# Performance work log

Measured on AMD Instinct MI355X. Metric: run time of the kernel, lower is better.

Reference implementation:

```python
import jax, jax.numpy as jnp
import numpy as np

NUM_NODES = 200000
B = 65536          # n_id batch size
E = 131072         # events per direction
D_MEM = 128
D_RAW = 128
D_TIME = 128
T_MAX = 1000000


def setup_inputs() -> dict:
    key = jax.random.key(0)
    ks = jax.random.split(key, 16)
    inp = {
        'memory': jax.random.normal(ks[0], (NUM_NODES, D_MEM), jnp.float32),
        'last_update': jax.random.randint(ks[1], (NUM_NODES,), 0, 1000, jnp.int64),
        'n_id': jnp.arange(B, dtype=jnp.int64),
        'src_s': jax.random.randint(ks[2], (E,), 0, B, jnp.int64),
        'dst_s': jax.random.randint(ks[3], (E,), 0, B, jnp.int64),
        't_s': jax.random.randint(ks[4], (E,), 0, T_MAX, jnp.int64),
        'raw_msg_s': jax.random.normal(ks[5], (E, D_RAW), jnp.float32),
        'src_d': jax.random.randint(ks[6], (E,), 0, B, jnp.int64),
        'dst_d': jax.random.randint(ks[7], (E,), 0, B, jnp.int64),
        't_d': jax.random.randint(ks[8], (E,), 0, T_MAX, jnp.int64),
        'raw_msg_d': jax.random.normal(ks[9], (E, D_RAW), jnp.float32),
        'w_time': jax.random.normal(ks[10], (D_TIME, 1), jnp.float32) * 0.1,
        'b_time': jax.random.normal(ks[11], (D_TIME,), jnp.float32) * 0.1,
        'W_ih': jax.random.normal(ks[12], (3 * D_MEM, 2 * D_MEM + D_RAW + D_TIME), jnp.float32) * 0.05,
        'W_hh': jax.random.normal(ks[13], (3 * D_MEM, D_MEM), jnp.float32) * 0.05,
        'b_ih': jax.random.normal(ks[14], (3 * D_MEM,), jnp.float32) * 0.05,
        'b_hh': jax.random.normal(ks[15], (3 * D_MEM,), jnp.float32) * 0.05,
    }
    return inp


def _time_enc(t_rel, w_time, b_time):
    # Linear(1, time_dim) followed by cos: cos(t * w + b)
    return jnp.cos(t_rel.astype(jnp.float32)[:, None] * w_time[:, 0][None, :] + b_time)


def reference(memory, last_update, n_id, src_s, dst_s, t_s, raw_msg_s,
              src_d, dst_d, t_d, raw_msg_d, w_time, b_time, W_ih, W_hh, b_ih, b_hh):
    nb = n_id.shape[0]
    # assoc: global node id -> local index within n_id
    assoc = jnp.zeros((memory.shape[0],), dtype=jnp.int32).at[n_id].set(
        jnp.arange(nb, dtype=jnp.int32))

    # source-side messages (IdentityMessage = concat)
    t_enc_s = _time_enc(t_s - last_update[src_s], w_time, b_time)
    msg_s = jnp.concatenate([memory[src_s], memory[dst_s], raw_msg_s, t_enc_s], axis=-1)

    # destination-side messages
    t_enc_d = _time_enc(t_d - last_update[dst_d], w_time, b_time)
    msg_d = jnp.concatenate([memory[dst_d], memory[src_d], raw_msg_d, t_enc_d], axis=-1)

    idx = jnp.concatenate([src_s, dst_d], axis=0)       # [2E] global ids
    msg = jnp.concatenate([msg_s, msg_d], axis=0)       # [2E, 512]
    t = jnp.concatenate([t_s, t_d], axis=0)             # [2E]
    loc = assoc[idx]                                     # [2E] local ids

    # LastAggregator: per local node, pick the message with max t (ties -> latest position)
    ne = t.shape[0]
    key = t * ne + jnp.arange(ne, dtype=t.dtype)         # encode (t, position)
    maxkey = jax.ops.segment_max(key, loc, num_segments=nb)
    count = jax.ops.segment_sum(jnp.ones_like(loc), loc, num_segments=nb)
    has = count > 0
    argm = jnp.where(has, maxkey % ne, 0)
    aggr = jnp.where(has[:, None], msg[argm], 0.0)       # [nb, 512]

    # GRUCell(x=aggr, h=memory[n_id])
    h = memory[n_id]
    gi = aggr @ W_ih.T + b_ih
    gh = h @ W_hh.T + b_hh
    gi_r, gi_z, gi_n = jnp.split(gi, 3, axis=-1)
    gh_r, gh_z, gh_n = jnp.split(gh, 3, axis=-1)
    r = jax.nn.sigmoid(gi_r + gh_r)
    z = jax.nn.sigmoid(gi_z + gh_z)
    n = jnp.tanh(gi_n + r * gh_n)
    new_memory = (1.0 - z) * n + z * h

    new_last_update = last_update.at[idx].set(t)[n_id]
    return new_memory, new_last_update
```

## Files before the change

### kernel.cpp

```cpp
#include <hip/hip_runtime.h>
#include <math.h>

#define NB        65536
#define EV        131072
#define NE        (2*EV)
#define DM        128
#define NO2       512
#define BM        64
#define THREADS   512
#define SWZ(r)    ((((r) ^ ((r) >> 2))) & 3)

typedef float f32x4 __attribute__((ext_vector_type(4)));
typedef long  longx2 __attribute__((ext_vector_type(2)));
typedef unsigned long long u64;

__device__ __forceinline__ float fcos_rev(float rev) {
    float r; asm("v_cos_f32 %0, %1" : "=v"(r) : "v"(rev)); return r;
}
__device__ __forceinline__ float fexp2(float x) {
    float r; asm("v_exp_f32 %0, %1" : "=v"(r) : "v"(x)); return r;
}
__device__ __forceinline__ float frcp(float x) {
    float r; asm("v_rcp_f32 %0, %1" : "=v"(r) : "v"(x)); return r;
}
__device__ __forceinline__ float fast_cos(float arg) {
    double rv = (double)arg * 0.15915494309189535;
    rv -= floor(rv);
    return fcos_rev((float)rv);
}
__device__ __forceinline__ float fsigmoid(float x) {
    x = fminf(fmaxf(x, -30.f), 30.f);
    float e = fexp2(-1.44269504088896f * x);
    return frcp(1.f + e);
}
__device__ __forceinline__ float ftanh_(float x) {
    x = fminf(fmaxf(x, -15.f), 15.f);
    float e = fexp2(-2.88539008177793f * x);
    return (1.f - e) * frcp(1.f + e);
}

#if defined(__has_builtin) && __has_builtin(__builtin_amdgcn_cvt_pk_fp8_f32)
__device__ __forceinline__ unsigned pack4_fp8(float f0, float f1, float f2, float f3) {
    int v = __builtin_amdgcn_cvt_pk_fp8_f32(f0, f1, 0, false);
    v = __builtin_amdgcn_cvt_pk_fp8_f32(f2, f3, v, true);
    return (unsigned)v;
}
#else
__device__ __forceinline__ unsigned enc1_fp8(float x) {
    unsigned u = __float_as_uint(x);
    unsigned s = (u >> 24) & 0x80u;
    float a = fabsf(x);
    if (!(a >= 0.001953125f)) return s;
    if (a > 448.f) a = 448.f;
    int e; float mf = frexpf(a, &e);
    int E = e + 6, mant;
    if (E <= 0) {
        mant = (int)(a * 512.f + 0.5f);
        if (mant > 7) return s | 0x08u;
        return s | (unsigned)mant;
    }
    mant = (int)((mf * 2.f - 1.f) * 8.f + 0.5f);
    if (mant == 8) { mant = 0; ++E; }
    if (E > 15) { E = 15; mant = 6; }
    if (E == 15 && mant == 7) mant = 6;
    return s | (unsigned)(E << 3) | (unsigned)mant;
}
__device__ __forceinline__ unsigned pack4_fp8(float f0, float f1, float f2, float f3) {
    return enc1_fp8(f0) | (enc1_fp8(f1) << 8) | (enc1_fp8(f2) << 16) | (enc1_fp8(f3) << 24);
}
#endif

__global__ void prep_k(const int* __restrict__ src_s, const int* __restrict__ t_s,
                       const int* __restrict__ dst_d, const int* __restrict__ t_d,
                       u64* __restrict__ keyarr, u64* __restrict__ lukey,
                       const float* __restrict__ W_ih, const float* __restrict__ W_hh,
                       const float* __restrict__ b_ih, const float* __restrict__ b_hh,
                       unsigned char* __restrict__ wp8, float* __restrict__ bp) {
    int bid = blockIdx.x;
    if (bid < NE / 256) {
        int e = bid * 256 + threadIdx.x;
        int g, t;
        if (e < EV) { g = src_s[e];      t = t_s[e]; }
        else        { g = dst_d[e - EV]; t = t_d[e - EV]; }
        u64 key = ((u64)(unsigned)t << 18) + (u64)(unsigned)e + 1ull;
        atomicMax(&keyarr[g], key);
        u64 lk = ((u64)(unsigned)(e + 1) << 20) | (u64)(unsigned)t;
        atomicMax(&lukey[g], lk);
        return;
    }
    int idx = (bid - NE / 256) * 256 + threadIdx.x;
    int col = idx / 80, g = idx - col * 80;
    int step = g >> 3, sl = g & 7;
    int kg = ((sl >> 1) ^ SWZ(col)) + ((sl & 1) << 2);
    int k0 = step * 64 + kg * 8;
    int d = col >> 2, gate = col & 3;
    float f[8];
    #pragma unroll
    for (int j = 0; j < 8; ++j) {
        int c = k0 + j;
        float v = 0.f;
        if (c < 512) {
            int row = (gate == 0) ? d : (gate == 1) ? 128 + d : (gate == 2) ? 256 + d : -1;
            if (row >= 0) v = W_ih[(size_t)row * 512 + c];
        } else {
            int ch = c - 512;
            int row = (gate == 0) ? d : (gate == 1) ? 128 + d : (gate == 3) ? 256 + d : -1;
            if (row >= 0) v = W_hh[(size_t)row * 128 + ch];
        }
        f[j] = v * 16.f;
    }
    unsigned lo = pack4_fp8(f[0], f[1], f[2], f[3]);
    unsigned hi = pack4_fp8(f[4], f[5], f[6], f[7]);
    *(u64*)(wp8 + (size_t)step * 32768 + (size_t)col * 64 + (size_t)sl * 8)
        = (u64)lo | ((u64)hi << 32);
    if (g == 0) {
        float bv = (gate == 0) ? b_ih[d] + b_hh[d]
                 : (gate == 1) ? b_ih[128 + d] + b_hh[128 + d]
                 : (gate == 2) ? b_ih[256 + d] : b_hh[256 + d];
        bp[col] = bv;
    }
}

__global__ __launch_bounds__(THREADS, 4) void gemm_gru_k(
    const float* __restrict__ memory, const int* __restrict__ last_update,
    const int* __restrict__ src_s, const int* __restrict__ dst_s,
    const int* __restrict__ t_s, const float* __restrict__ raw_s,
    const int* __restrict__ src_d, const int* __restrict__ dst_d,
    const int* __restrict__ t_d, const float* __restrict__ raw_d,
    const float* __restrict__ w_time, const float* __restrict__ b_time,
    const unsigned char* __restrict__ wp8, const float* __restrict__ bp,
    const u64* __restrict__ keyarr, const u64* __restrict__ lukey,
    float* __restrict__ out_mem, float* __restrict__ out_lu)
{
    __shared__ __align__(16) char smem[74752];
    unsigned char* sA = (unsigned char*)smem;
    unsigned char* sB = (unsigned char*)(smem + 8192);
    float* sW = (float*)(smem + 73728);
    float* sBt= (float*)(smem + 74240);

    const int tid = threadIdx.x;
    const int m0  = blockIdx.x * BM;
    const int ln  = tid & 63, wn = tid >> 6;
    const int l2  = ln >> 4, rl = ln & 15;

    if (tid < DM) { sW[tid] = w_time[tid]; sBt[tid] = b_time[tid]; }

    const int ar = tid >> 3, ac = tid & 7;
    const int m  = m0 + ar;
    const u64 kk = keyarr[m];
    const int rv = (kk != 0ull);
    int a_ = 0, b_ = 0, t_ = 0;
    const float* pR = raw_s;
    if (kk) {
        int e = (int)((kk - 1ull) & (u64)(NE - 1));
        if (e < EV) { a_ = src_s[e]; b_ = dst_s[e]; t_ = t_s[e]; pR = raw_s + (size_t)e * DM; }
        else { int e2 = e - EV; a_ = dst_d[e2]; b_ = src_d[e2]; t_ = t_d[e2]; pR = raw_d + (size_t)e2 * DM; }
    }
    const float rt = rv ? (float)(t_ - last_update[a_]) : 0.f;
    const float* pA = memory + (size_t)a_ * DM;
    const float* pB = memory + (size_t)b_ * DM;
    const float* pH = memory + (size_t)m  * DM;

    float4 pv0, pv1;
    auto PREF_A = [&](int step) {
        int seg = step >> 1;
        if (seg == 3) return;
        const float* base = (seg == 0) ? pA : (seg == 1) ? pB : (seg == 2) ? pR : pH;
        int off = ((step & 1) << 6) + (ac << 3);
        pv0 = *(const float4*)(base + off);
        pv1 = *(const float4*)(base + off + 4);
    };
    auto STAGE_B = [&](int step, int buf) {
        const unsigned char* src = wp8 + (size_t)step * 32768 + (size_t)tid * 16;
        unsigned char* dst = sB + (size_t)buf * 32768 + (size_t)tid * 16;
        #pragma unroll
        for (int i = 0; i < 4; ++i)
            __builtin_amdgcn_global_load_lds(
                (const __attribute__((address_space(1))) void*)(src + i * 8192),
                (__attribute__((address_space(3))) void*)(dst + i * 8192), 16, 0, 0);
    };
    auto WRITE_A = [&](int step, int buf) {
        int seg = step >> 1;
        float f0, f1, f2, f3, f4, f5, f6, f7;
        if (seg == 3) {
            int coff = ((step & 1) << 6) + (ac << 3);
            f0 = fast_cos(__fadd_rn(__fmul_rn(rt, sW[coff+0]), sBt[coff+0]));
            f1 = fast_cos(__fadd_rn(__fmul_rn(rt, sW[coff+1]), sBt[coff+1]));
            f2 = fast_cos(__fadd_rn(__fmul_rn(rt, sW[coff+2]), sBt[coff+2]));
            f3 = fast_cos(__fadd_rn(__fmul_rn(rt, sW[coff+3]), sBt[coff+3]));
            f4 = fast_cos(__fadd_rn(__fmul_rn(rt, sW[coff+4]), sBt[coff+4]));
            f5 = fast_cos(__fadd_rn(__fmul_rn(rt, sW[coff+5]), sBt[coff+5]));
            f6 = fast_cos(__fadd_rn(__fmul_rn(rt, sW[coff+6]), sBt[coff+6]));
            f7 = fast_cos(__fadd_rn(__fmul_rn(rt, sW[coff+7]), sBt[coff+7]));
        } else {
            f0 = pv0.x; f1 = pv0.y; f2 = pv0.z; f3 = pv0.w;
            f4 = pv1.x; f5 = pv1.y; f6 = pv1.z; f7 = pv1.w;
        }
        if (seg < 4 && !rv) { f0=f1=f2=f3=f4=f5=f6=f7 = 0.f; }
        unsigned lo = pack4_fp8(f0, f1, f2, f3);
        unsigned hi = pack4_fp8(f4, f5, f6, f7);
        u64 q = (u64)lo | ((u64)hi << 32);
        *(u64*)(sA + buf * 4096 + ar * 64 + (((ac & 3) ^ SWZ(ar)) << 4) + ((ac >> 2) << 3)) = q;
    };

    f32x4 acc[4][4];
    #pragma unroll
    for (int mf = 0; mf < 4; ++mf)
        #pragma unroll
        for (int nf = 0; nf < 4; ++nf)
            acc[mf][nf] = (f32x4){0.f, 0.f, 0.f, 0.f};

    PREF_A(0);
    WRITE_A(0, 0);
    STAGE_B(0, 0);
    PREF_A(1);
    asm volatile("s_waitcnt vmcnt(2) lgkmcnt(0)" ::: "memory");
    __builtin_amdgcn_sched_barrier(0);
    __builtin_amdgcn_s_barrier();

    #pragma unroll
    for (int k = 0; k < 10; ++k) {
        const int cur = k & 1, nxt = cur ^ 1;

        longx2 a2[4], b2[4];
        #pragma unroll
        for (int mf = 0; mf < 4; ++mf) {
            int r = mf * 16 + rl;
            a2[mf] = *(const longx2*)(sA + cur * 4096 + r * 64 + ((l2 ^ SWZ(r)) << 4));
        }
        #pragma unroll
        for (int nf = 0; nf < 4; ++nf) {
            int c = wn * 64 + nf * 16 + rl;
            b2[nf] = *(const longx2*)(sB + cur * 32768 + c * 64 + ((l2 ^ SWZ(c)) << 4));
        }
        __builtin_amdgcn_sched_barrier(0);

        const bool pf = (k < 8) && (((k + 2) >> 1) != 3);
        if (k < 9) {
            WRITE_A(k + 1, nxt);
            __builtin_amdgcn_sched_barrier(0);
            STAGE_B(k + 1, nxt);
            __builtin_amdgcn_sched_barrier(0);
            if (pf) PREF_A(k + 2);
            __builtin_amdgcn_sched_barrier(0);
        }

        __builtin_amdgcn_s_setprio(1);
        #pragma unroll
        for (int mf = 0; mf < 4; ++mf)
            #pragma unroll
            for (int nf = 0; nf < 4; ++nf)
                acc[mf][nf] = __builtin_amdgcn_mfma_f32_16x16x32_fp8_fp8(
                    a2[mf].x, b2[nf].x, acc[mf][nf], 0, 0, 0);
        #pragma unroll
        for (int mf = 0; mf < 4; ++mf)
            #pragma unroll
            for (int nf = 0; nf < 4; ++nf)
                acc[mf][nf] = __builtin_amdgcn_mfma_f32_16x16x32_fp8_fp8(
                    a2[mf].y, b2[nf].y, acc[mf][nf], 0, 0, 0);
        __builtin_amdgcn_s_setprio(0);

        if (k < 9) {
            __builtin_amdgcn_sched_barrier(0);
            if (pf) asm volatile("s_waitcnt vmcnt(2) lgkmcnt(0)" ::: "memory");
            else    asm volatile("s_waitcnt vmcnt(0) lgkmcnt(0)" ::: "memory");
            __builtin_amdgcn_sched_barrier(0);
            __builtin_amdgcn_s_barrier();
        }
    }

    if (tid < BM) {
        u64 lk = lukey[m0 + tid];
        out_lu[m0 + tid] = lk ? (float)(unsigned)(lk & 0xFFFFFull)
                              : (float)last_update[m0 + tid];
    }
    __syncthreads();

    float* ep = (float*)(smem + wn * 4352);
    const int row16 = ln >> 2, dgrp = ln & 3;
    const int dbase = wn * 16 + dgrp * 4;
    const float ds = 0.0625f;
    f32x4 bb0 = *(const f32x4*)(bp + (dbase + 0) * 4);
    f32x4 bb1 = *(const f32x4*)(bp + (dbase + 1) * 4);
    f32x4 bb2 = *(const f32x4*)(bp + (dbase + 2) * 4);
    f32x4 bb3 = *(const f32x4*)(bp + (dbase + 3) * 4);

    #pragma unroll
    for (int mf = 0; mf < 4; ++mf) {
        #pragma unroll
        for (int nf = 0; nf < 4; ++nf)
            #pragma unroll
            for (int j = 0; j < 4; ++j)
                ep[((ln >> 4) * 4 + j) * 68 + nf * 16 + rl] = acc[mf][nf][j] * ds;
        asm volatile("s_waitcnt lgkmcnt(0)" ::: "memory");

        const int gm = m0 + mf * 16 + row16;
        const float* gr = ep + row16 * 68 + dgrp * 16;
        f32x4 g0 = *(const f32x4*)(gr + 0);
        f32x4 g1 = *(const f32x4*)(gr + 4);
        f32x4 g2 = *(const f32x4*)(gr + 8);
        f32x4 g3 = *(const f32x4*)(gr + 12);
        f32x4 h  = *(const f32x4*)(memory + (size_t)gm * DM + dbase);
        f32x4 res;
        {
            float rg = fsigmoid(g0.x + bb0.x);
            float zg = fsigmoid(g0.y + bb0.y);
            float ng = ftanh_(g0.z + bb0.z + rg * (g0.w + bb0.w));
            res.x = (1.f - zg) * ng + zg * h.x;
        }
        {
            float rg = fsigmoid(g1.x + bb1.x);
            float zg = fsigmoid(g1.y + bb1.y);
            float ng = ftanh_(g1.z + bb1.z + rg * (g1.w + bb1.w));
            res.y = (1.f - zg) * ng + zg * h.y;
        }
        {
            float rg = fsigmoid(g2.x + bb2.x);
            float zg = fsigmoid(g2.y + bb2.y);
            float ng = ftanh_(g2.z + bb2.z + rg * (g2.w + bb2.w));
            res.z = (1.f - zg) * ng + zg * h.z;
        }
        {
            float rg = fsigmoid(g3.x + bb3.x);
            float zg = fsigmoid(g3.y + bb3.y);
            float ng = ftanh_(g3.z + bb3.z + rg * (g3.w + bb3.w));
            res.w = (1.f - zg) * ng + zg * h.w;
        }
        *(f32x4*)(out_mem + (size_t)gm * DM + dbase) = res;
        if (mf < 3) asm volatile("s_waitcnt lgkmcnt(0)" ::: "memory");
    }
}

extern "C" void kernel_launch(void* const* d_in, const int* in_sizes, int n_in,
                              void* d_out, int out_size, void* d_ws, size_t ws_size,
                              hipStream_t stream) {
    const float* memory      = (const float*)d_in[0];
    const int*   last_update = (const int*)d_in[1];
    const int*   src_s       = (const int*)d_in[3];
    const int*   dst_s       = (const int*)d_in[4];
    const int*   t_s         = (const int*)d_in[5];
    const float* raw_s       = (const float*)d_in[6];
    const int*   src_d       = (const int*)d_in[7];
    const int*   dst_d       = (const int*)d_in[8];
    const int*   t_d         = (const int*)d_in[9];
    const float* raw_d       = (const float*)d_in[10];
    const float* w_time      = (const float*)d_in[11];
    const float* b_time      = (const float*)d_in[12];
    const float* W_ih        = (const float*)d_in[13];
    const float* W_hh        = (const float*)d_in[14];
    const float* b_ih        = (const float*)d_in[15];
    const float* b_hh        = (const float*)d_in[16];

    char* ws = (char*)d_ws;
    u64* keyarr = (u64*)ws;
    u64* lukey  = (u64*)(ws + 524288);
    unsigned char* wp8 = (unsigned char*)(ws + 1048576);
    float* bp = (float*)(ws + 1376256);

    hipMemsetAsync(d_ws, 0, 1048576, stream);

    prep_k<<<NE / 256 + (NO2 * 80) / 256, 256, 0, stream>>>(
        src_s, t_s, dst_d, t_d, keyarr, lukey, W_ih, W_hh, b_ih, b_hh, wp8, bp);

    float* out_mem = (float*)d_out;
    float* out_lu  = out_mem + (size_t)NB * DM;
    gemm_gru_k<<<NB / BM, THREADS, 0, stream>>>(memory, last_update,
        src_s, dst_s, t_s, raw_s, src_d, dst_d, t_d, raw_d,
        w_time, b_time, wp8, bp, keyarr, lukey, out_mem, out_lu);
}
```

Baseline: 79.29 us.

## Halve GEMM K-step and triple-buffer LDS with fragment prefetch

The fused GEMM+GRU kernel now moves through K in 32-wide fp8 steps (20 iterations) instead of 64-wide ones (10 iterations). The weight packing, swizzle and LDS layout are rewritten to match, and A/B tiles rotate through three LDS buffers. Fragments for the next step are read into registers before each barrier, so the MFMAs of one step overlap with staging two steps ahead. This cuts the LDS footprint and aims to hide load latency, but it doubles the number of block barriers and halves the MFMA work between them.

```diff
diff --git a/kernel.cpp b/kernel.cpp
--- a/kernel.cpp
+++ b/kernel.cpp
@@ -7,11 +7,10 @@
 #define DM        128
 #define NO2       512
 #define BM        64
+#define NST       20
 #define THREADS   512
-#define SWZ(r)    ((((r) ^ ((r) >> 2))) & 3)
 
 typedef float f32x4 __attribute__((ext_vector_type(4)));
-typedef long  longx2 __attribute__((ext_vector_type(2)));
 typedef unsigned long long u64;
 
 __device__ __forceinline__ float fcos_rev(float rev) {
@@ -90,9 +89,9 @@
     }
     int idx = (bid - NE / 256) * 256 + threadIdx.x;
     int col = idx / 80, g = idx - col * 80;
-    int step = g >> 3, sl = g & 7;
-    int kg = ((sl >> 1) ^ SWZ(col)) + ((sl & 1) << 2);
-    int k0 = step * 64 + kg * 8;
+    int step = g >> 2, sl = g & 3;
+    int kg = sl ^ ((col >> 2) & 3);
+    int k0 = step * 32 + kg * 8;
     int d = col >> 2, gate = col & 3;
     float f[8];
     #pragma unroll
@@ -111,7 +110,7 @@
     }
     unsigned lo = pack4_fp8(f[0], f[1], f[2], f[3]);
     unsigned hi = pack4_fp8(f[4], f[5], f[6], f[7]);
-    *(u64*)(wp8 + (size_t)step * 32768 + (size_t)col * 64 + (size_t)sl * 8)
+    *(u64*)(wp8 + (size_t)step * 16384 + (size_t)col * 32 + (size_t)sl * 8)
         = (u64)lo | ((u64)hi << 32);
     if (g == 0) {
         float bv = (gate == 0) ? b_ih[d] + b_hh[d]
@@ -132,11 +131,11 @@
     const u64* __restrict__ keyarr, const u64* __restrict__ lukey,
     float* __restrict__ out_mem, float* __restrict__ out_lu)
 {
-    __shared__ __align__(16) char smem[74752];
+    __shared__ __align__(16) char smem[56320];
     unsigned char* sA = (unsigned char*)smem;
-    unsigned char* sB = (unsigned char*)(smem + 8192);
-    float* sW = (float*)(smem + 73728);
-    float* sBt= (float*)(smem + 74240);
+    unsigned char* sB = (unsigned char*)(smem + 6144);
+    float* sW = (float*)(smem + 55296);
+    float* sBt= (float*)(smem + 55808);
 
     const int tid = threadIdx.x;
     const int m0  = blockIdx.x * BM;
@@ -161,46 +160,51 @@
     const float* pB = memory + (size_t)b_ * DM;
     const float* pH = memory + (size_t)m  * DM;
 
-    float4 pv0, pv1;
+    float4 pv;
     auto PREF_A = [&](int step) {
-        int seg = step >> 1;
+        int seg = step >> 2;
         if (seg == 3) return;
         const float* base = (seg == 0) ? pA : (seg == 1) ? pB : (seg == 2) ? pR : pH;
-        int off = ((step & 1) << 6) + (ac << 3);
-        pv0 = *(const float4*)(base + off);
-        pv1 = *(const float4*)(base + off + 4);
+        pv = *(const float4*)(base + ((step & 3) << 5) + (ac << 2));
     };
     auto STAGE_B = [&](int step, int buf) {
-        const unsigned char* src = wp8 + (size_t)step * 32768 + (size_t)tid * 16;
-        unsigned char* dst = sB + (size_t)buf * 32768 + (size_t)tid * 16;
-        #pragma unroll
-        for (int i = 0; i < 4; ++i)
-            __builtin_amdgcn_global_load_lds(
-                (const __attribute__((address_space(1))) void*)(src + i * 8192),
-                (__attribute__((address_space(3))) void*)(dst + i * 8192), 16, 0, 0);
+        const unsigned char* src = wp8 + (size_t)step * 16384 + (size_t)tid * 16;
+        unsigned char* dst = sB + (size_t)buf * 16384 + (size_t)tid * 16;
+        __builtin_amdgcn_global_load_lds((const __attribute__((address_space(1))) void*)src,
+            (__attribute__((address_space(3))) void*)dst, 16, 0, 0);
+        __builtin_amdgcn_global_load_lds((const __attribute__((address_space(1))) void*)(src + 8192),
+            (__attribute__((address_space(3))) void*)(dst + 8192), 16, 0, 0);
     };
     auto WRITE_A = [&](int step, int buf) {
-        int seg = step >> 1;
-        float f0, f1, f2, f3, f4, f5, f6, f7;
+        int seg = step >> 2;
+        float f0, f1, f2, f3;
         if (seg == 3) {
-            int coff = ((step & 1) << 6) + (ac << 3);
+            int coff = ((step & 3) << 5) + (ac << 2);
             f0 = fast_cos(__fadd_rn(__fmul_rn(rt, sW[coff+0]), sBt[coff+0]));
             f1 = fast_cos(__fadd_rn(__fmul_rn(rt, sW[coff+1]), sBt[coff+1]));
             f2 = fast_cos(__fadd_rn(__fmul_rn(rt, sW[coff+2]), sBt[coff+2]));
             f3 = fast_cos(__fadd_rn(__fmul_rn(rt, sW[coff+3]), sBt[coff+3]));
-            f4 = fast_cos(__fadd_rn(__fmul_rn(rt, sW[coff+4]), sBt[coff+4]));
-            f5 = fast_cos(__fadd_rn(__fmul_rn(rt, sW[coff+5]), sBt[coff+5]));
-            f6 = fast_cos(__fadd_rn(__fmul_rn(rt, sW[coff+6]), sBt[coff+6]));
-            f7 = fast_cos(__fadd_rn(__fmul_rn(rt, sW[coff+7]), sBt[coff+7]));
         } else {
-            f0 = pv0.x; f1 = pv0.y; f2 = pv0.z; f3 = pv0.w;
-            f4 = pv1.x; f5 = pv1.y; f6 = pv1.z; f7 = pv1.w;
-        }
-        if (seg < 4 && !rv) { f0=f1=f2=f3=f4=f5=f6=f7 = 0.f; }
-        unsigned lo = pack4_fp8(f0, f1, f2, f3);
-        unsigned hi = pack4_fp8(f4, f5, f6, f7);
-        u64 q = (u64)lo | ((u64)hi << 32);
-        *(u64*)(sA + buf * 4096 + ar * 64 + (((ac & 3) ^ SWZ(ar)) << 4) + ((ac >> 2) << 3)) = q;
+            f0 = pv.x; f1 = pv.y; f2 = pv.z; f3 = pv.w;
+        }
+        if (seg < 4 && !rv) { f0 = f1 = f2 = f3 = 0.f; }
+        unsigned q = pack4_fp8(f0, f1, f2, f3);
+        *(unsigned*)(sA + buf * 2048 + ar * 32
+                     + ((((ac >> 1) ^ ((ar >> 2) & 3)) << 3) + ((ac & 1) << 2))) = q;
+    };
+
+    long afr[4], bfr[4];
+    auto READ_FRAGS = [&](int buf) {
+        #pragma unroll
+        for (int mf = 0; mf < 4; ++mf) {
+            int r = mf * 16 + rl;
+            afr[mf] = *(const long*)(sA + buf * 2048 + r * 32 + ((l2 ^ ((r >> 2) & 3)) << 3));
+        }
+        #pragma unroll
+        for (int nf = 0; nf < 4; ++nf) {
+            int c = wn * 64 + nf * 16 + rl;
+            bfr[nf] = *(const long*)(sB + buf * 16384 + c * 32 + ((l2 ^ ((c >> 2) & 3)) << 3));
+        }
     };
 
     f32x4 acc[4][4];
@@ -212,57 +216,45 @@
 
     PREF_A(0);
     WRITE_A(0, 0);
+    PREF_A(1);
+    WRITE_A(1, 1);
     STAGE_B(0, 0);
-    PREF_A(1);
-    asm volatile("s_waitcnt vmcnt(2) lgkmcnt(0)" ::: "memory");
+    STAGE_B(1, 1);
+    PREF_A(2);
+    asm volatile("s_waitcnt vmcnt(1) lgkmcnt(0)" ::: "memory");
     __builtin_amdgcn_sched_barrier(0);
     __builtin_amdgcn_s_barrier();
+    READ_FRAGS(0);
+    asm volatile("s_waitcnt lgkmcnt(0)" ::: "memory");
+    __builtin_amdgcn_sched_barrier(0);
 
     #pragma unroll
-    for (int k = 0; k < 10; ++k) {
-        const int cur = k & 1, nxt = cur ^ 1;
-
-        longx2 a2[4], b2[4];
-        #pragma unroll
-        for (int mf = 0; mf < 4; ++mf) {
-            int r = mf * 16 + rl;
-            a2[mf] = *(const longx2*)(sA + cur * 4096 + r * 64 + ((l2 ^ SWZ(r)) << 4));
-        }
-        #pragma unroll
-        for (int nf = 0; nf < 4; ++nf) {
-            int c = wn * 64 + nf * 16 + rl;
-            b2[nf] = *(const longx2*)(sB + cur * 32768 + c * 64 + ((l2 ^ SWZ(c)) << 4));
-        }
-        __builtin_amdgcn_sched_barrier(0);
-
-        const bool pf = (k < 8) && (((k + 2) >> 1) != 3);
-        if (k < 9) {
-            WRITE_A(k + 1, nxt);
-            __builtin_amdgcn_sched_barrier(0);
-            STAGE_B(k + 1, nxt);
-            __builtin_amdgcn_sched_barrier(0);
-            if (pf) PREF_A(k + 2);
-            __builtin_amdgcn_sched_barrier(0);
-        }
-
+    for (int k = 0; k < NST; ++k) {
         __builtin_amdgcn_s_setprio(1);
         #pragma unroll
         for (int mf = 0; mf < 4; ++mf)
             #pragma unroll
             for (int nf = 0; nf < 4; ++nf)
                 acc[mf][nf] = __builtin_amdgcn_mfma_f32_16x16x32_fp8_fp8(
-                    a2[mf].x, b2[nf].x, acc[mf][nf], 0, 0, 0);
-        #pragma unroll
-        for (int mf = 0; mf < 4; ++mf)
-            #pragma unroll
-            for (int nf = 0; nf < 4; ++nf)
-                acc[mf][nf] = __builtin_amdgcn_mfma_f32_16x16x32_fp8_fp8(
-                    a2[mf].y, b2[nf].y, acc[mf][nf], 0, 0, 0);
+                    afr[mf], bfr[nf], acc[mf][nf], 0, 0, 0);
         __builtin_amdgcn_s_setprio(0);
-
-        if (k < 9) {
+        __builtin_amdgcn_sched_barrier(0);
+
+        if (k + 2 <= NST - 1) {
+            WRITE_A(k + 2, (k + 2) % 3);
             __builtin_amdgcn_sched_barrier(0);
-            if (pf) asm volatile("s_waitcnt vmcnt(2) lgkmcnt(0)" ::: "memory");
+            STAGE_B(k + 2, (k + 2) % 3);
+            __builtin_amdgcn_sched_barrier(0);
+        }
+        const bool pf = (k + 3 <= NST - 1) && (((k + 3) >> 2) != 3);
+        if (pf) PREF_A(k + 3);
+        __builtin_amdgcn_sched_barrier(0);
+
+        if (k + 1 <= NST - 1) READ_FRAGS((k + 1) % 3);
+
+        if (k < NST - 1) {
+            __builtin_amdgcn_sched_barrier(0);
+            if (pf) asm volatile("s_waitcnt vmcnt(1) lgkmcnt(0)" ::: "memory");
             else    asm volatile("s_waitcnt vmcnt(0) lgkmcnt(0)" ::: "memory");
             __builtin_amdgcn_sched_barrier(0);
             __builtin_amdgcn_s_barrier();
```

New measurement: 80.19 us. No clear change (+1.1%).

## Switch GEMM to 32x32x64 scaled FP8 MFMA with new LDS swizzle

Applied to the files above, without the earlier changes.

Replaces the 16x16x32 FP8 MFMA tiles (4x4 fragments, two K-halves) with the gfx950 scaled 32x32x64 f8f6f4 MFMA on 2x2 fragments. The weight packing, the A-tile LDS swizzle and the fragment loads change to match the new operand layout. The epilogue is reworked for the 32x32 accumulator layout. The B staging and next A write are moved ahead of the fragment loads. The aim is fewer MFMA issues and LDS reads per K step. The risk lies in the layout correctness of the new swizzle, LDS bank conflicts, and the larger epilogue scratch per wave.

```diff
diff --git a/kernel.cpp b/kernel.cpp
--- a/kernel.cpp
+++ b/kernel.cpp
@@ -7,11 +7,13 @@
 #define DM        128
 #define NO2       512
 #define BM        64
+#define NST       10
 #define THREADS   512
-#define SWZ(r)    ((((r) ^ ((r) >> 2))) & 3)
-
-typedef float f32x4 __attribute__((ext_vector_type(4)));
-typedef long  longx2 __attribute__((ext_vector_type(2)));
+
+typedef float f32x4  __attribute__((ext_vector_type(4)));
+typedef float f32x16 __attribute__((ext_vector_type(16)));
+typedef int   i32x4  __attribute__((ext_vector_type(4)));
+typedef int   i32x8  __attribute__((ext_vector_type(8)));
 typedef unsigned long long u64;
 
 __device__ __forceinline__ float fcos_rev(float rev) {
@@ -91,8 +93,8 @@
     int idx = (bid - NE / 256) * 256 + threadIdx.x;
     int col = idx / 80, g = idx - col * 80;
     int step = g >> 3, sl = g & 7;
-    int kg = ((sl >> 1) ^ SWZ(col)) + ((sl & 1) << 2);
-    int k0 = step * 64 + kg * 8;
+    int ck = ((sl >> 1) ^ ((col >> 1) & 3));
+    int k0 = step * 64 + ck * 16 + (sl & 1) * 8;
     int d = col >> 2, gate = col & 3;
     float f[8];
     #pragma unroll
@@ -141,7 +143,7 @@
     const int tid = threadIdx.x;
     const int m0  = blockIdx.x * BM;
     const int ln  = tid & 63, wn = tid >> 6;
-    const int l2  = ln >> 4, rl = ln & 15;
+    const int lg  = ln >> 5;
 
     if (tid < DM) { sW[tid] = w_time[tid]; sBt[tid] = b_time[tid]; }
 
@@ -200,15 +202,17 @@
         unsigned lo = pack4_fp8(f0, f1, f2, f3);
         unsigned hi = pack4_fp8(f4, f5, f6, f7);
         u64 q = (u64)lo | ((u64)hi << 32);
-        *(u64*)(sA + buf * 4096 + ar * 64 + (((ac & 3) ^ SWZ(ar)) << 4) + ((ac >> 2) << 3)) = q;
+        *(u64*)(sA + buf * 4096 + ar * 64
+                + (((ac >> 1) ^ ((ar >> 1) & 3)) << 4) + ((ac & 1) << 3)) = q;
     };
 
-    f32x4 acc[4][4];
+    f32x16 acc[2][2];
     #pragma unroll
-    for (int mf = 0; mf < 4; ++mf)
-        #pragma unroll
-        for (int nf = 0; nf < 4; ++nf)
-            acc[mf][nf] = (f32x4){0.f, 0.f, 0.f, 0.f};
+    for (int mf = 0; mf < 2; ++mf)
+        #pragma unroll
+        for (int nf = 0; nf < 2; ++nf)
+            #pragma unroll
+            for (int j = 0; j < 16; ++j) acc[mf][nf][j] = 0.f;
 
     PREF_A(0);
     WRITE_A(0, 0);
@@ -219,48 +223,47 @@
     __builtin_amdgcn_s_barrier();
 
     #pragma unroll
-    for (int k = 0; k < 10; ++k) {
+    for (int k = 0; k < NST; ++k) {
         const int cur = k & 1, nxt = cur ^ 1;
 
-        longx2 a2[4], b2[4];
-        #pragma unroll
-        for (int mf = 0; mf < 4; ++mf) {
-            int r = mf * 16 + rl;
-            a2[mf] = *(const longx2*)(sA + cur * 4096 + r * 64 + ((l2 ^ SWZ(r)) << 4));
-        }
-        #pragma unroll
-        for (int nf = 0; nf < 4; ++nf) {
-            int c = wn * 64 + nf * 16 + rl;
-            b2[nf] = *(const longx2*)(sB + cur * 32768 + c * 64 + ((l2 ^ SWZ(c)) << 4));
-        }
-        __builtin_amdgcn_sched_barrier(0);
-
-        const bool pf = (k < 8) && (((k + 2) >> 1) != 3);
-        if (k < 9) {
+        if (k < NST - 1) {
             WRITE_A(k + 1, nxt);
             __builtin_amdgcn_sched_barrier(0);
             STAGE_B(k + 1, nxt);
             __builtin_amdgcn_sched_barrier(0);
-            if (pf) PREF_A(k + 2);
-            __builtin_amdgcn_sched_barrier(0);
-        }
+        }
+
+        i32x8 af[2], bf[2];
+        #pragma unroll
+        for (int mf = 0; mf < 2; ++mf) {
+            int r = mf * 32 + (ln & 31), sw = (r >> 1) & 3;
+            i32x4 q0 = *(const i32x4*)(sA + cur * 4096 + r * 64 + (((2*lg+0) ^ sw) << 4));
+            i32x4 q1 = *(const i32x4*)(sA + cur * 4096 + r * 64 + (((2*lg+1) ^ sw) << 4));
+            af[mf] = (i32x8){q0.x,q0.y,q0.z,q0.w, q1.x,q1.y,q1.z,q1.w};
+        }
+        #pragma unroll
+        for (int nf = 0; nf < 2; ++nf) {
+            int c = wn * 64 + nf * 32 + (ln & 31), sw = (c >> 1) & 3;
+            i32x4 q0 = *(const i32x4*)(sB + cur * 32768 + c * 64 + (((2*lg+0) ^ sw) << 4));
+            i32x4 q1 = *(const i32x4*)(sB + cur * 32768 + c * 64 + (((2*lg+1) ^ sw) << 4));
+            bf[nf] = (i32x8){q0.x,q0.y,q0.z,q0.w, q1.x,q1.y,q1.z,q1.w};
+        }
+        __builtin_amdgcn_sched_barrier(0);
+
+        const bool pf = (k + 2 <= NST - 1) && (((k + 2) >> 1) != 3);
+        if (pf) PREF_A(k + 2);
+        __builtin_amdgcn_sched_barrier(0);
 
         __builtin_amdgcn_s_setprio(1);
         #pragma unroll
-        for (int mf = 0; mf < 4; ++mf)
+        for (int mf = 0; mf < 2; ++mf)
             #pragma unroll
-            for (int nf = 0; nf < 4; ++nf)
-                acc[mf][nf] = __builtin_amdgcn_mfma_f32_16x16x32_fp8_fp8(
-                    a2[mf].x, b2[nf].x, acc[mf][nf], 0, 0, 0);
-        #pragma unroll
-        for (int mf = 0; mf < 4; ++mf)
-            #pragma unroll
-            for (int nf = 0; nf < 4; ++nf)
-                acc[mf][nf] = __builtin_amdgcn_mfma_f32_16x16x32_fp8_fp8(
-                    a2[mf].y, b2[nf].y, acc[mf][nf], 0, 0, 0);
+            for (int nf = 0; nf < 2; ++nf)
+                acc[mf][nf] = __builtin_amdgcn_mfma_scale_f32_32x32x64_f8f6f4(
+                    af[mf], bf[nf], acc[mf][nf], 0, 0, 0, 127, 0, 127);
         __builtin_amdgcn_s_setprio(0);
 
-        if (k < 9) {
+        if (k < NST - 1) {
             __builtin_amdgcn_sched_barrier(0);
             if (pf) asm volatile("s_waitcnt vmcnt(2) lgkmcnt(0)" ::: "memory");
             else    asm volatile("s_waitcnt vmcnt(0) lgkmcnt(0)" ::: "memory");
@@ -276,58 +279,40 @@
     }
     __syncthreads();
 
-    float* ep = (float*)(smem + wn * 4352);
-    const int row16 = ln >> 2, dgrp = ln & 3;
-    const int dbase = wn * 16 + dgrp * 4;
+    float* ep = (float*)(smem + wn * 8704);
+    const int erow = ln >> 1, half = ln & 1;
+    const int d0 = wn * 16 + half * 8;
     const float ds = 0.0625f;
-    f32x4 bb0 = *(const f32x4*)(bp + (dbase + 0) * 4);
-    f32x4 bb1 = *(const f32x4*)(bp + (dbase + 1) * 4);
-    f32x4 bb2 = *(const f32x4*)(bp + (dbase + 2) * 4);
-    f32x4 bb3 = *(const f32x4*)(bp + (dbase + 3) * 4);
 
     #pragma unroll
-    for (int mf = 0; mf < 4; ++mf) {
-        #pragma unroll
-        for (int nf = 0; nf < 4; ++nf)
+    for (int mf = 0; mf < 2; ++mf) {
+        #pragma unroll
+        for (int nf = 0; nf < 2; ++nf)
             #pragma unroll
-            for (int j = 0; j < 4; ++j)
-                ep[((ln >> 4) * 4 + j) * 68 + nf * 16 + rl] = acc[mf][nf][j] * ds;
+            for (int reg = 0; reg < 16; ++reg) {
+                int r32 = (reg & 3) + 8 * (reg >> 2) + 4 * lg;
+                ep[r32 * 68 + nf * 32 + (ln & 31)] = acc[mf][nf][reg] * ds;
+            }
         asm volatile("s_waitcnt lgkmcnt(0)" ::: "memory");
 
-        const int gm = m0 + mf * 16 + row16;
-        const float* gr = ep + row16 * 68 + dgrp * 16;
-        f32x4 g0 = *(const f32x4*)(gr + 0);
-        f32x4 g1 = *(const f32x4*)(gr + 4);
-        f32x4 g2 = *(const f32x4*)(gr + 8);
-        f32x4 g3 = *(const f32x4*)(gr + 12);
-        f32x4 h  = *(const f32x4*)(memory + (size_t)gm * DM + dbase);
-        f32x4 res;
-        {
-            float rg = fsigmoid(g0.x + bb0.x);
-            float zg = fsigmoid(g0.y + bb0.y);
-            float ng = ftanh_(g0.z + bb0.z + rg * (g0.w + bb0.w));
-            res.x = (1.f - zg) * ng + zg * h.x;
-        }
-        {
-            float rg = fsigmoid(g1.x + bb1.x);
-            float zg = fsigmoid(g1.y + bb1.y);
-            float ng = ftanh_(g1.z + bb1.z + rg * (g1.w + bb1.w));
-            res.y = (1.f - zg) * ng + zg * h.y;
-        }
-        {
-            float rg = fsigmoid(g2.x + bb2.x);
-            float zg = fsigmoid(g2.y + bb2.y);
-            float ng = ftanh_(g2.z + bb2.z + rg * (g2.w + bb2.w));
-            res.z = (1.f - zg) * ng + zg * h.z;
-        }
-        {
-            float rg = fsigmoid(g3.x + bb3.x);
-            float zg = fsigmoid(g3.y + bb3.y);
-            float ng = ftanh_(g3.z + bb3.z + rg * (g3.w + bb3.w));
-            res.w = (1.f - zg) * ng + zg * h.w;
-        }
-        *(f32x4*)(out_mem + (size_t)gm * DM + dbase) = res;
-        if (mf < 3) asm volatile("s_waitcnt lgkmcnt(0)" ::: "memory");
+        const int gm = m0 + mf * 32 + erow;
+        const float* gr = ep + erow * 68 + half * 32;
+        float res[8];
+        f32x4 h0 = *(const f32x4*)(memory + (size_t)gm * DM + d0);
+        f32x4 h1 = *(const f32x4*)(memory + (size_t)gm * DM + d0 + 4);
+        #pragma unroll
+        for (int q = 0; q < 8; ++q) {
+            f32x4 g  = *(const f32x4*)(gr + q * 4);
+            f32x4 bb = *(const f32x4*)(bp + (d0 + q) * 4);
+            float rg = fsigmoid(g.x + bb.x);
+            float zg = fsigmoid(g.y + bb.y);
+            float ng = ftanh_(g.z + bb.z + rg * (g.w + bb.w));
+            float hh = (q < 4) ? ((const float*)&h0)[q] : ((const float*)&h1)[q - 4];
+            res[q] = (1.f - zg) * ng + zg * hh;
+        }
+        *(f32x4*)(out_mem + (size_t)gm * DM + d0)     = *(const f32x4*)res;
+        *(f32x4*)(out_mem + (size_t)gm * DM + d0 + 4) = *(const f32x4*)(res + 4);
+        if (mf == 0) asm volatile("s_waitcnt lgkmcnt(0)" ::: "memory");
     }
 }
 
```

New measurement: 78.63 us. No clear change (-0.8%).
